# Optimization experiments

Hardware: AMD Instinct MI355X
Metric: run time of the kernel (lower is better)

Reference implementation:

```python
import jax, jax.numpy as jnp
import numpy as np

B, L, D = 2048, 100, 128          # batch, early_cycle_threshold, d_model
F = L * D                          # flattened curve features = 12800
DLLM, DFF, E, K = 768, 256, 8, 2   # d_llm, d_ff, num_experts, top_k
EPS = 1e-9


def setup_inputs() -> dict:
    key = jax.random.key(0)
    ks = jax.random.split(key, 12)
    gin = DLLM + 1 + F  # gate input dim: concat(DKP, cycle_number, flat curve)
    return {
        "cycle_curve_data": jax.random.normal(ks[0], (B, L, D), jnp.float32),
        "cycle_numbers": jax.random.uniform(ks[1], (B, 1), jnp.float32) * 100.0,
        "DKP_embeddings": jax.random.normal(ks[2], (B, DLLM), jnp.float32),
        # gate MLP (PatternRouter_three): concat -> d_ff -> gelu -> num_experts
        "Wg1": jax.random.normal(ks[3], (gin, DFF), jnp.float32) / np.sqrt(gin),
        "bg1": jnp.zeros((DFF,), jnp.float32),
        "Wg2": jax.random.normal(ks[4], (DFF, E), jnp.float32) / np.sqrt(DFF),
        "bg2": jnp.zeros((E,), jnp.float32),
        # per-expert Linear(F, d_model)
        "We": jax.random.normal(ks[5], (E, F, D), jnp.float32) / np.sqrt(F),
        "be": jnp.zeros((E, D), jnp.float32),
        # general expert Linear(F, d_model)
        "Wgen": jax.random.normal(ks[6], (F, D), jnp.float32) / np.sqrt(F),
        "bgen": jnp.zeros((D,), jnp.float32),
    }


def reference(cycle_curve_data, cycle_numbers, DKP_embeddings,
              Wg1, bg1, Wg2, bg2, We, be, Wgen, bgen):
    b = cycle_curve_data.shape[0]
    xf = cycle_curve_data.reshape(b, -1)  # [B, F]

    # gate logits: MLP on concat(DKP, cycle_numbers, flattened curve)
    gin = jnp.concatenate([DKP_embeddings, cycle_numbers, xf], axis=-1)
    h = jax.nn.gelu(gin @ Wg1 + bg1)
    logits = h @ Wg2 + bg2                # [B, E]

    # top-k mask, softmax over ALL experts, then mask + renormalize
    _, idx = jax.lax.top_k(logits, K)     # [B, K]
    mask = jnp.sum(jax.nn.one_hot(idx, E, dtype=logits.dtype), axis=1)  # [B, E]
    probs = jax.nn.softmax(logits, axis=-1)
    masked = probs * mask
    gates = masked / (jnp.sum(masked, axis=-1, keepdims=True) + EPS)  # [B, E]

    # experts: dense compute, zero gates nullify unselected experts (same math
    # as gather-compute-scatter dispatch/combine)
    expert_outs = jnp.einsum('bf,efd->bed', xf, We) + be   # [B, E, D]
    combined = jnp.einsum('be,bed->bd', gates, expert_outs)
    combined = combined.astype(jnp.bfloat16)               # torch .to(bfloat16)

    general = xf @ Wgen + bgen                              # [B, D] f32
    final_out = general + combined.astype(general.dtype)    # bf16+f32 -> f32
    return final_out
```

## Files before the change

kernel.cpp:

```cpp
#include <hip/hip_runtime.h>
#include <hip/hip_bf16.h>
#include <stdint.h>

#define B_    2048
#define F_    12800
#define DLLM_ 768
#define DFF_  256
#define E_    8
#define GIN_K (DLLM_ + F_)
#define G1Z   32
#define MKSPLIT 8
#define MKPER (F_ / MKSPLIT)
#define BK    64

typedef __bf16 bf16x8 __attribute__((ext_vector_type(8)));
typedef float  f32x4  __attribute__((ext_vector_type(4)));

__device__ __forceinline__ unsigned short f2bf(float f) {
    unsigned int u = __float_as_uint(f);
    u += 0x7fffu + ((u >> 16) & 1u);
    return (unsigned short)(u >> 16);
}

__global__ __launch_bounds__(256) void k_convert(const float* __restrict__ src,
                                                 unsigned short* __restrict__ dst, int n4) {
    int i = blockIdx.x * 256 + threadIdx.x;
    if (i >= n4) return;
    float4 v = ((const float4*)src)[i];
    ushort4 o;
    o.x = f2bf(v.x); o.y = f2bf(v.y); o.z = f2bf(v.z); o.w = f2bf(v.w);
    ((ushort4*)dst)[i] = o;
}

__global__ __launch_bounds__(256) void k_transpose_bf16(const float* __restrict__ We,
                                                        const float* __restrict__ Wgen,
                                                        unsigned short* __restrict__ WeT,
                                                        unsigned short* __restrict__ WgenT) {
    __shared__ float t[32][33];
    int z = blockIdx.z;
    const float* src = (z < 8) ? (We + (size_t)z * F_ * 128) : Wgen;
    unsigned short* dst = (z < 8) ? (WeT + (size_t)z * 128 * F_) : WgenT;
    int k0 = blockIdx.x * 32, n0 = blockIdx.y * 32;
    int tx = threadIdx.x, ty = threadIdx.y;
#pragma unroll
    for (int i = 0; i < 4; i++) {
        int k = k0 + ty + i * 8;
        t[ty + i * 8][tx] = src[(size_t)k * 128 + n0 + tx];
    }
    __syncthreads();
#pragma unroll
    for (int i = 0; i < 4; i++) {
        int n = n0 + ty + i * 8;
        dst[(size_t)n * F_ + k0 + tx] = f2bf(t[tx][ty + i * 8]);
    }
}

__global__ __launch_bounds__(256) void k_gate1(const float* __restrict__ dkp,
                                               const float* __restrict__ xf,
                                               const float* __restrict__ Wg1,
                                               float* __restrict__ h_pre) {
    __shared__ float As[16][132];
    __shared__ float Bs[16][132];
    int m0 = blockIdx.x * 128;
    int n0 = blockIdx.y * 128;
    int s = blockIdx.z;
    int it0 = s * 26 + (s < 16 ? s : 16);
    int nit = 26 + (s < 16 ? 1 : 0);
    int kbeg = it0 * 16, kend = kbeg + nit * 16;
    int t = threadIdx.x;
    int tx = t & 15, ty = t >> 4;

    float acc[8][8];
#pragma unroll
    for (int i = 0; i < 8; i++)
#pragma unroll
        for (int j = 0; j < 8; j++) acc[i][j] = 0.f;

    int lm = t >> 2;
    int lkq = (t & 3) * 4;
    int br = t >> 5;
    int bc = (t & 31) * 4;

    float4 aReg[2], bReg[2];
    auto preload = [&](int k) {
        const float* Ab; int astr, aoff, wr0;
        if (k < DLLM_) { Ab = dkp; astr = DLLM_; aoff = k; wr0 = k; }
        else           { Ab = xf;  astr = F_;    aoff = k - DLLM_; wr0 = k + 1; }
#pragma unroll
        for (int p = 0; p < 2; p++)
            aReg[p] = *(const float4*)&Ab[(size_t)(m0 + p * 64 + lm) * astr + aoff + lkq];
#pragma unroll
        for (int p = 0; p < 2; p++)
            bReg[p] = *(const float4*)&Wg1[(size_t)(wr0 + p * 8 + br) * 256 + n0 + bc];
    };
    preload(kbeg);
    for (int k = kbeg; k < kend; k += 16) {
        __syncthreads();
#pragma unroll
        for (int p = 0; p < 2; p++) {
            As[lkq + 0][p * 64 + lm] = aReg[p].x;
            As[lkq + 1][p * 64 + lm] = aReg[p].y;
            As[lkq + 2][p * 64 + lm] = aReg[p].z;
            As[lkq + 3][p * 64 + lm] = aReg[p].w;
            *(float4*)&Bs[p * 8 + br][bc] = bReg[p];
        }
        __syncthreads();
        if (k + 16 < kend) preload(k + 16);
#pragma unroll
        for (int kk = 0; kk < 16; kk++) {
            float4 a0 = *(const float4*)&As[kk][ty * 4];
            float4 a1 = *(const float4*)&As[kk][64 + ty * 4];
            float4 b0 = *(const float4*)&Bs[kk][tx * 4];
            float4 b1 = *(const float4*)&Bs[kk][64 + tx * 4];
            float av[8] = {a0.x, a0.y, a0.z, a0.w, a1.x, a1.y, a1.z, a1.w};
            float bv[8] = {b0.x, b0.y, b0.z, b0.w, b1.x, b1.y, b1.z, b1.w};
#pragma unroll
            for (int i = 0; i < 8; i++)
#pragma unroll
                for (int j = 0; j < 8; j++) acc[i][j] = fmaf(av[i], bv[j], acc[i][j]);
        }
    }
#pragma unroll
    for (int i = 0; i < 8; i++) {
        int row = m0 + ((i < 4) ? (ty * 4 + i) : (64 + ty * 4 + i - 4));
#pragma unroll
        for (int j = 0; j < 8; j++) {
            int col = n0 + ((j < 4) ? (tx * 4 + j) : (64 + tx * 4 + j - 4));
            atomicAdd(&h_pre[(size_t)row * 256 + col], acc[i][j]);
        }
    }
}

__global__ __launch_bounds__(256) void k_gate2(const float* __restrict__ h_pre,
                                               const float* __restrict__ cyc,
                                               const float* __restrict__ Wg1,
                                               const float* __restrict__ bg1,
                                               const float* __restrict__ Wg2,
                                               const float* __restrict__ bg2,
                                               float* __restrict__ gates,
                                               unsigned int* __restrict__ cnt,
                                               unsigned int* __restrict__ rows) {
    __shared__ float hs[8 * 257];
    __shared__ float w2s[256 * 8];
    __shared__ float ls[8][9];
    int r0 = blockIdx.x * 8;
    int t = threadIdx.x;
    const float* w768 = Wg1 + (size_t)DLLM_ * 256;
    float wc = w768[t], b1c = bg1[t];
#pragma unroll
    for (int i = 0; i < 8; i++) {
        float x = h_pre[(size_t)(r0 + i) * 256 + t] + cyc[r0 + i] * wc + b1c;
        float x3 = x * x * x;
        float g = 0.5f * x * (1.f + tanhf(0.7978845608028654f * (x + 0.044715f * x3)));
        hs[i * 257 + t] = g;
    }
#pragma unroll
    for (int i = 0; i < 8; i++) w2s[i * 256 + t] = Wg2[i * 256 + t];
    __syncthreads();
    if (t < 64) {
        int r = t >> 3, e = t & 7;
        float s = bg2[e];
        for (int k2 = 0; k2 < 256; k2++) s = fmaf(hs[r * 257 + k2], w2s[k2 * 8 + e], s);
        ls[r][e] = s;
    }
    __syncthreads();
    if (t < 8) {
        float l[8];
#pragma unroll
        for (int e = 0; e < 8; e++) l[e] = ls[t][e];
        int i1 = 0; float v1 = l[0];
#pragma unroll
        for (int e = 1; e < 8; e++) if (l[e] > v1) { v1 = l[e]; i1 = e; }
        int i2 = -1; float v2 = -3.0e38f;
#pragma unroll
        for (int e = 0; e < 8; e++) if (e != i1 && l[e] > v2) { v2 = l[e]; i2 = e; }
        float p[8], ps = 0.f;
#pragma unroll
        for (int e = 0; e < 8; e++) { p[e] = expf(l[e] - v1); ps += p[e]; }
        float msum = (p[i1] + p[i2]) / ps;
        float gi = 1.f / (msum + 1e-9f);
        int row = r0 + t;
#pragma unroll
        for (int e = 0; e < 8; e++) {
            float ge = (e == i1 || e == i2) ? (p[e] / ps) * gi : 0.f;
            gates[row * 8 + e] = ge;
        }
        unsigned int s1 = atomicAdd(&cnt[i1], 1u); rows[i1 * 2048 + s1] = (unsigned int)row;
        unsigned int s2 = atomicAdd(&cnt[i2], 1u); rows[i2 * 2048 + s2] = (unsigned int)row;
    }
}

__global__ __launch_bounds__(256) void k_moe(const unsigned short* __restrict__ xfb,
                                             const unsigned short* __restrict__ WeT,
                                             const unsigned short* __restrict__ WgenT,
                                             const float* __restrict__ be,
                                             const float* __restrict__ gates,
                                             const unsigned int* __restrict__ cnt,
                                             const unsigned int* __restrict__ rows,
                                             float* __restrict__ comb,
                                             float* __restrict__ gen) {
    __shared__ unsigned short As[64 * 72];
    __shared__ unsigned short Bs[128 * 72];
    __shared__ unsigned int rowid_s[64];
    int e = blockIdx.y, tile = blockIdx.x, split = blockIdx.z;
    int n_rows = (e < 8) ? (int)cnt[e] : 2048;
    if (tile * 64 >= n_rows) return;
    int t = threadIdx.x;
    if (t < 64) {
        int m = tile * 64 + t;
        unsigned int row = (e < 8) ? ((m < n_rows) ? rows[e * 2048 + m] : rows[e * 2048])
                                   : (unsigned int)m;
        rowid_s[t] = row;
    }
    __syncthreads();
    const unsigned short* WT = (e < 8) ? (WeT + (size_t)e * 128 * F_) : WgenT;
    int k0 = split * MKPER;

    int arow = t >> 2, akq = t & 3;
    const unsigned short* aptr = xfb + (size_t)rowid_s[arow] * F_ + k0 + akq * 8;
    unsigned short* asd0 = &As[arow * 72 + akq * 8];
    unsigned short* asd1 = &As[arow * 72 + (akq + 4) * 8];
    int bcol = t >> 1, bh = t & 1;
    const unsigned short* bptr = WT + (size_t)bcol * F_ + k0 + bh * 32;
    unsigned short* bsd = &Bs[bcol * 72 + bh * 32];

    int lane = t & 63;
    int lm = lane & 15, lg = lane >> 4;
    int wave = t >> 6, wr = wave >> 1, wc2 = wave & 1;

    f32x4 acc[2][4];
#pragma unroll
    for (int i = 0; i < 2; i++)
#pragma unroll
        for (int j = 0; j < 4; j++) acc[i][j] = (f32x4){0.f, 0.f, 0.f, 0.f};

    uint4 ra0 = *(const uint4*)aptr;
    uint4 ra1 = *(const uint4*)(aptr + 32);
    uint4 rb0 = *(const uint4*)(bptr);
    uint4 rb1 = *(const uint4*)(bptr + 8);
    uint4 rb2 = *(const uint4*)(bptr + 16);
    uint4 rb3 = *(const uint4*)(bptr + 24);
    for (int kk = 0; kk < MKPER; kk += BK) {
        __syncthreads();
        *(uint4*)asd0 = ra0;
        *(uint4*)asd1 = ra1;
        *(uint4*)(bsd)      = rb0;
        *(uint4*)(bsd + 8)  = rb1;
        *(uint4*)(bsd + 16) = rb2;
        *(uint4*)(bsd + 24) = rb3;
        __syncthreads();
        if (kk + BK < MKPER) {
            aptr += BK; bptr += BK;
            ra0 = *(const uint4*)aptr;
            ra1 = *(const uint4*)(aptr + 32);
            rb0 = *(const uint4*)(bptr);
            rb1 = *(const uint4*)(bptr + 8);
            rb2 = *(const uint4*)(bptr + 16);
            rb3 = *(const uint4*)(bptr + 24);
        }
#pragma unroll
        for (int kb = 0; kb < 2; kb++) {
            bf16x8 af[2], bfr[4];
#pragma unroll
            for (int mt = 0; mt < 2; mt++)
                af[mt] = *(const bf16x8*)&As[(wr * 32 + mt * 16 + lm) * 72 + (kb * 4 + lg) * 8];
#pragma unroll
            for (int nt = 0; nt < 4; nt++)
                bfr[nt] = *(const bf16x8*)&Bs[(wc2 * 64 + nt * 16 + lm) * 72 + (kb * 4 + lg) * 8];
#pragma unroll
            for (int mt = 0; mt < 2; mt++)
#pragma unroll
                for (int nt = 0; nt < 4; nt++)
                    acc[mt][nt] = __builtin_amdgcn_mfma_f32_16x16x32_bf16(af[mt], bfr[nt], acc[mt][nt], 0, 0, 0);
        }
    }
#pragma unroll
    for (int mt = 0; mt < 2; mt++) {
        int rl0 = wr * 32 + mt * 16 + lg * 4;
#pragma unroll
        for (int nt = 0; nt < 4; nt++) {
            int col = wc2 * 64 + nt * 16 + lm;
#pragma unroll
            for (int r = 0; r < 4; r++) {
                int rloc = rl0 + r;
                float v = acc[mt][nt][r];
                if (e < 8) {
                    if (tile * 64 + rloc < n_rows) {
                        unsigned int grow = rowid_s[rloc];
                        float g = gates[grow * 8 + e];
                        float bias = (split == 0) ? be[e * 128 + col] : 0.f;
                        atomicAdd(&comb[(size_t)grow * 128 + col], g * (v + bias));
                    }
                } else {
                    atomicAdd(&gen[(size_t)(tile * 64 + rloc) * 128 + col], v);
                }
            }
        }
    }
}

__global__ __launch_bounds__(256) void k_final(const float* __restrict__ gen,
                                               const float* __restrict__ comb,
                                               const float* __restrict__ bgen,
                                               float* __restrict__ out) {
    int i = blockIdx.x * 256 + threadIdx.x;
    float g = gen[i] + bgen[i & 127];
    unsigned short cb = f2bf(comb[i]);
    float c = __uint_as_float(((unsigned int)cb) << 16);
    out[i] = g + c;
}

extern "C" void kernel_launch(void* const* d_in, const int* in_sizes, int n_in,
                              void* d_out, int out_size, void* d_ws, size_t ws_size,
                              hipStream_t stream) {
    (void)in_sizes; (void)n_in; (void)out_size; (void)ws_size;
    const float* ccd  = (const float*)d_in[0];
    const float* cyc  = (const float*)d_in[1];
    const float* dkp  = (const float*)d_in[2];
    const float* Wg1  = (const float*)d_in[3];
    const float* bg1  = (const float*)d_in[4];
    const float* Wg2  = (const float*)d_in[5];
    const float* bg2  = (const float*)d_in[6];
    const float* We   = (const float*)d_in[7];
    const float* be   = (const float*)d_in[8];
    const float* Wgen = (const float*)d_in[9];
    const float* bgen = (const float*)d_in[10];
    float* out = (float*)d_out;

    char* ws = (char*)d_ws;
    size_t o = 0;
    unsigned short* xfb   = (unsigned short*)(ws + o); o += (size_t)B_ * F_ * 2;
    unsigned short* WeT   = (unsigned short*)(ws + o); o += (size_t)E_ * 128 * F_ * 2;
    unsigned short* WgenT = (unsigned short*)(ws + o); o += (size_t)128 * F_ * 2;
    float* h_pre = (float*)(ws + o); o += (size_t)B_ * 256 * 4;
    float* gates = (float*)(ws + o); o += (size_t)B_ * 8 * 4;
    unsigned int* cnt = (unsigned int*)(ws + o); o += 256;
    unsigned int* rows = (unsigned int*)(ws + o); o += (size_t)8 * 2048 * 4;
    float* comb = (float*)(ws + o); o += (size_t)B_ * 128 * 4;
    float* gen  = (float*)(ws + o); o += (size_t)B_ * 128 * 4;

    hipMemsetAsync(h_pre, 0, (size_t)B_ * 256 * 4, stream);
    hipMemsetAsync(comb, 0, (size_t)B_ * 128 * 4, stream);
    hipMemsetAsync(gen,  0, (size_t)B_ * 128 * 4, stream);
    hipMemsetAsync(cnt,  0, 32, stream);

    k_convert<<<(B_ * F_ / 4) / 256, 256, 0, stream>>>(ccd, xfb, B_ * F_ / 4);
    k_transpose_bf16<<<dim3(F_ / 32, 4, 9), dim3(32, 8, 1), 0, stream>>>(We, Wgen, WeT, WgenT);
    k_gate1<<<dim3(16, 2, G1Z), 256, 0, stream>>>(dkp, ccd, Wg1, h_pre);
    k_gate2<<<B_ / 8, 256, 0, stream>>>(h_pre, cyc, Wg1, bg1, Wg2, bg2, gates, cnt, rows);
    k_moe<<<dim3(32, 9, MKSPLIT), 256, 0, stream>>>(xfb, WeT, WgenT, be, gates, cnt, rows, comb, gen);
    k_final<<<(B_ * 128) / 256, 256, 0, stream>>>(gen, comb, bgen, out);
}
```

Baseline: 762.9 us.

## Widen gate GEMM tile to full N and replace atomics with partial-sum buffers

The gate1 FP32 GEMM now covers all 256 output columns per block with a 128x256 tile, each thread holding 16x8 accumulators, so each A tile is loaded from global memory once instead of twice. When the workspace is large enough, split-K partials are written with plain vector stores into per-split buffers and summed in gate2, avoiding float atomics and the memset. The tradeoffs are higher register pressure (launch bounds set to 2 blocks), half as many blocks, an extra 64MB partial buffer that gate2 must read back, and a dependence on the workspace size.

```diff
diff --git a/kernel.cpp b/kernel.cpp
--- a/kernel.cpp
+++ b/kernel.cpp
@@ -5,9 +5,7 @@
 #define B_    2048
 #define F_    12800
 #define DLLM_ 768
-#define DFF_  256
 #define E_    8
-#define GIN_K (DLLM_ + F_)
 #define G1Z   32
 #define MKSPLIT 8
 #define MKPER (F_ / MKSPLIT)
@@ -55,83 +53,94 @@
     }
 }
 
-__global__ __launch_bounds__(256) void k_gate1(const float* __restrict__ dkp,
-                                               const float* __restrict__ xf,
-                                               const float* __restrict__ Wg1,
-                                               float* __restrict__ h_pre) {
+__global__ __launch_bounds__(256, 2) void k_gate1(const float* __restrict__ dkp,
+                                                  const float* __restrict__ xf,
+                                                  const float* __restrict__ Wg1,
+                                                  float* __restrict__ h_part,
+                                                  int nparts) {
     __shared__ float As[16][132];
-    __shared__ float Bs[16][132];
+    __shared__ float Bs[16][260];
     int m0 = blockIdx.x * 128;
-    int n0 = blockIdx.y * 128;
-    int s = blockIdx.z;
+    int s = blockIdx.y;
     int it0 = s * 26 + (s < 16 ? s : 16);
     int nit = 26 + (s < 16 ? 1 : 0);
-    int kbeg = it0 * 16, kend = kbeg + nit * 16;
     int t = threadIdx.x;
-    int tx = t & 15, ty = t >> 4;
-
-    float acc[8][8];
-#pragma unroll
-    for (int i = 0; i < 8; i++)
+    int tm = t >> 5;
+    int tn = t & 31;
+
+    float acc[16][8];
+#pragma unroll
+    for (int i = 0; i < 16; i++)
 #pragma unroll
         for (int j = 0; j < 8; j++) acc[i][j] = 0.f;
 
-    int lm = t >> 2;
-    int lkq = (t & 3) * 4;
-    int br = t >> 5;
-    int bc = (t & 31) * 4;
-
-    float4 aReg[2], bReg[2];
+    int arow = t >> 2, akq = (t & 3) * 4;
+    int bkr = t >> 6, bcol = (t & 63) * 4;
+
+    float4 aR[2], bR[4];
     auto preload = [&](int k) {
         const float* Ab; int astr, aoff, wr0;
         if (k < DLLM_) { Ab = dkp; astr = DLLM_; aoff = k; wr0 = k; }
         else           { Ab = xf;  astr = F_;    aoff = k - DLLM_; wr0 = k + 1; }
-#pragma unroll
-        for (int p = 0; p < 2; p++)
-            aReg[p] = *(const float4*)&Ab[(size_t)(m0 + p * 64 + lm) * astr + aoff + lkq];
-#pragma unroll
-        for (int p = 0; p < 2; p++)
-            bReg[p] = *(const float4*)&Wg1[(size_t)(wr0 + p * 8 + br) * 256 + n0 + bc];
+        aR[0] = *(const float4*)&Ab[(size_t)(m0 + arow) * astr + aoff + akq];
+        aR[1] = *(const float4*)&Ab[(size_t)(m0 + arow + 64) * astr + aoff + akq];
+#pragma unroll
+        for (int r = 0; r < 4; r++)
+            bR[r] = *(const float4*)&Wg1[(size_t)(wr0 + bkr + r * 4) * 256 + bcol];
     };
-    preload(kbeg);
-    for (int k = kbeg; k < kend; k += 16) {
+    preload(it0 * 16);
+    for (int it = 0; it < nit; it++) {
         __syncthreads();
-#pragma unroll
-        for (int p = 0; p < 2; p++) {
-            As[lkq + 0][p * 64 + lm] = aReg[p].x;
-            As[lkq + 1][p * 64 + lm] = aReg[p].y;
-            As[lkq + 2][p * 64 + lm] = aReg[p].z;
-            As[lkq + 3][p * 64 + lm] = aReg[p].w;
-            *(float4*)&Bs[p * 8 + br][bc] = bReg[p];
+        {
+            float a0[4] = {aR[0].x, aR[0].y, aR[0].z, aR[0].w};
+            float a1[4] = {aR[1].x, aR[1].y, aR[1].z, aR[1].w};
+#pragma unroll
+            for (int j = 0; j < 4; j++) {
+                As[akq + j][arow]      = a0[j];
+                As[akq + j][arow + 64] = a1[j];
+            }
+#pragma unroll
+            for (int r = 0; r < 4; r++)
+                *(float4*)&Bs[bkr + r * 4][bcol] = bR[r];
         }
         __syncthreads();
-        if (k + 16 < kend) preload(k + 16);
-#pragma unroll
+        if (it + 1 < nit) preload((it0 + it + 1) * 16);
+#pragma unroll 4
         for (int kk = 0; kk < 16; kk++) {
-            float4 a0 = *(const float4*)&As[kk][ty * 4];
-            float4 a1 = *(const float4*)&As[kk][64 + ty * 4];
-            float4 b0 = *(const float4*)&Bs[kk][tx * 4];
-            float4 b1 = *(const float4*)&Bs[kk][64 + tx * 4];
-            float av[8] = {a0.x, a0.y, a0.z, a0.w, a1.x, a1.y, a1.z, a1.w};
-            float bv[8] = {b0.x, b0.y, b0.z, b0.w, b1.x, b1.y, b1.z, b1.w};
-#pragma unroll
-            for (int i = 0; i < 8; i++)
+            float4 a0 = *(const float4*)&As[kk][tm * 16];
+            float4 a1 = *(const float4*)&As[kk][tm * 16 + 4];
+            float4 a2 = *(const float4*)&As[kk][tm * 16 + 8];
+            float4 a3 = *(const float4*)&As[kk][tm * 16 + 12];
+            float4 b0 = *(const float4*)&Bs[kk][tn * 8];
+            float4 b1 = *(const float4*)&Bs[kk][tn * 8 + 4];
+            float av[16] = {a0.x, a0.y, a0.z, a0.w, a1.x, a1.y, a1.z, a1.w,
+                            a2.x, a2.y, a2.z, a2.w, a3.x, a3.y, a3.z, a3.w};
+            float bv[8]  = {b0.x, b0.y, b0.z, b0.w, b1.x, b1.y, b1.z, b1.w};
+#pragma unroll
+            for (int i = 0; i < 16; i++)
 #pragma unroll
                 for (int j = 0; j < 8; j++) acc[i][j] = fmaf(av[i], bv[j], acc[i][j]);
         }
     }
-#pragma unroll
-    for (int i = 0; i < 8; i++) {
-        int row = m0 + ((i < 4) ? (ty * 4 + i) : (64 + ty * 4 + i - 4));
-#pragma unroll
-        for (int j = 0; j < 8; j++) {
-            int col = n0 + ((j < 4) ? (tx * 4 + j) : (64 + tx * 4 + j - 4));
-            atomicAdd(&h_pre[(size_t)row * 256 + col], acc[i][j]);
-        }
-    }
-}
-
-__global__ __launch_bounds__(256) void k_gate2(const float* __restrict__ h_pre,
+    if (nparts > 1) {
+        float* dst = h_part + (size_t)s * B_ * 256;
+#pragma unroll
+        for (int i = 0; i < 16; i++) {
+            size_t base = (size_t)(m0 + tm * 16 + i) * 256 + tn * 8;
+            *(float4*)&dst[base]     = (float4){acc[i][0], acc[i][1], acc[i][2], acc[i][3]};
+            *(float4*)&dst[base + 4] = (float4){acc[i][4], acc[i][5], acc[i][6], acc[i][7]};
+        }
+    } else {
+#pragma unroll
+        for (int i = 0; i < 16; i++) {
+            size_t base = (size_t)(m0 + tm * 16 + i) * 256 + tn * 8;
+#pragma unroll
+            for (int j = 0; j < 8; j++) atomicAdd(&h_part[base + j], acc[i][j]);
+        }
+    }
+}
+
+__global__ __launch_bounds__(256) void k_gate2(const float* __restrict__ h_part,
                                                const float* __restrict__ cyc,
                                                const float* __restrict__ Wg1,
                                                const float* __restrict__ bg1,
@@ -139,7 +148,8 @@
                                                const float* __restrict__ bg2,
                                                float* __restrict__ gates,
                                                unsigned int* __restrict__ cnt,
-                                               unsigned int* __restrict__ rows) {
+                                               unsigned int* __restrict__ rows,
+                                               int nparts) {
     __shared__ float hs[8 * 257];
     __shared__ float w2s[256 * 8];
     __shared__ float ls[8][9];
@@ -149,7 +159,10 @@
     float wc = w768[t], b1c = bg1[t];
 #pragma unroll
     for (int i = 0; i < 8; i++) {
-        float x = h_pre[(size_t)(r0 + i) * 256 + t] + cyc[r0 + i] * wc + b1c;
+        size_t idx = (size_t)(r0 + i) * 256 + t;
+        float x = 0.f;
+        for (int p = 0; p < nparts; p++) x += h_part[(size_t)p * B_ * 256 + idx];
+        x += cyc[r0 + i] * wc + b1c;
         float x3 = x * x * x;
         float g = 0.5f * x * (1.f + tanhf(0.7978845608028654f * (x + 0.044715f * x3)));
         hs[i * 257 + t] = g;
@@ -313,7 +326,7 @@
 extern "C" void kernel_launch(void* const* d_in, const int* in_sizes, int n_in,
                               void* d_out, int out_size, void* d_ws, size_t ws_size,
                               hipStream_t stream) {
-    (void)in_sizes; (void)n_in; (void)out_size; (void)ws_size;
+    (void)in_sizes; (void)n_in; (void)out_size;
     const float* ccd  = (const float*)d_in[0];
     const float* cyc  = (const float*)d_in[1];
     const float* dkp  = (const float*)d_in[2];
@@ -332,22 +345,25 @@
     unsigned short* xfb   = (unsigned short*)(ws + o); o += (size_t)B_ * F_ * 2;
     unsigned short* WeT   = (unsigned short*)(ws + o); o += (size_t)E_ * 128 * F_ * 2;
     unsigned short* WgenT = (unsigned short*)(ws + o); o += (size_t)128 * F_ * 2;
-    float* h_pre = (float*)(ws + o); o += (size_t)B_ * 256 * 4;
     float* gates = (float*)(ws + o); o += (size_t)B_ * 8 * 4;
     unsigned int* cnt = (unsigned int*)(ws + o); o += 256;
     unsigned int* rows = (unsigned int*)(ws + o); o += (size_t)8 * 2048 * 4;
     float* comb = (float*)(ws + o); o += (size_t)B_ * 128 * 4;
     float* gen  = (float*)(ws + o); o += (size_t)B_ * 128 * 4;
-
-    hipMemsetAsync(h_pre, 0, (size_t)B_ * 256 * 4, stream);
+    float* h_part = (float*)(ws + o);
+    size_t need_full = o + (size_t)G1Z * B_ * 256 * 4;
+    int nparts = (ws_size >= need_full) ? G1Z : 1;
+
+    if (nparts == 1)
+        hipMemsetAsync(h_part, 0, (size_t)B_ * 256 * 4, stream);
     hipMemsetAsync(comb, 0, (size_t)B_ * 128 * 4, stream);
     hipMemsetAsync(gen,  0, (size_t)B_ * 128 * 4, stream);
     hipMemsetAsync(cnt,  0, 32, stream);
 
     k_convert<<<(B_ * F_ / 4) / 256, 256, 0, stream>>>(ccd, xfb, B_ * F_ / 4);
     k_transpose_bf16<<<dim3(F_ / 32, 4, 9), dim3(32, 8, 1), 0, stream>>>(We, Wgen, WeT, WgenT);
-    k_gate1<<<dim3(16, 2, G1Z), 256, 0, stream>>>(dkp, ccd, Wg1, h_pre);
-    k_gate2<<<B_ / 8, 256, 0, stream>>>(h_pre, cyc, Wg1, bg1, Wg2, bg2, gates, cnt, rows);
+    k_gate1<<<dim3(16, G1Z), 256, 0, stream>>>(dkp, ccd, Wg1, h_part, nparts);
+    k_gate2<<<B_ / 8, 256, 0, stream>>>(h_part, cyc, Wg1, bg1, Wg2, bg2, gates, cnt, rows, nparts);
     k_moe<<<dim3(32, 9, MKSPLIT), 256, 0, stream>>>(xfb, WeT, WgenT, be, gates, cnt, rows, comb, gen);
     k_final<<<(B_ * 128) / 256, 256, 0, stream>>>(gen, comb, bgen, out);
 }
```

New measurement: 652.1 us. 1.17x faster.
